# Optimization experiments

Hardware: AMD Instinct MI355X
Metric: run time of the kernel (lower is better)

## Reference

```python
import jax, jax.numpy as jnp
import numpy as np

B, DS, DM = 4, 64, 4096
NE, S = 1024, 2048


def setup_inputs() -> dict:
    key = jax.random.key(0)
    ks = jax.random.split(key, 9)
    std = 0.02
    return {
        "state": jax.random.normal(ks[0], (B, DS, DM), jnp.float32),
        "evicted_tokens": jax.random.normal(ks[1], (B, NE, DM), jnp.float32),
        "current_tokens": jax.random.normal(ks[2], (B, S, DM), jnp.float32),
        "W_key": std * jax.random.normal(ks[3], (DS, DM), jnp.float32),
        "W_beta_w": std * jax.random.normal(ks[4], (DS, DM), jnp.float32),
        "W_beta_b": jnp.zeros((DS,), jnp.float32),
        "W_query": std * jax.random.normal(ks[5], (DS, DM), jnp.float32),
        "gate_w": std * jax.random.normal(ks[6], (1, DM), jnp.float32),
        "gate_b": jnp.full((1,), -2.0, jnp.float32),  # gate_bias init
    }


def reference(state, evicted_tokens, current_tokens, W_key, W_beta_w, W_beta_b,
              W_query, gate_w, gate_b):
    # ---- compress: fold evicted tokens into SSM state ----
    # keys: [B, NE, DS]; softmax over the token axis (dim=1)
    keys = jnp.einsum('bnd,sd->bns', evicted_tokens, W_key)
    write_weights = jax.nn.softmax(keys, axis=1)
    # update: [B, DS, DM] = write_weights^T @ evicted_tokens
    update = jnp.einsum('bns,bnd->bsd', write_weights, evicted_tokens)
    summary = evicted_tokens.mean(axis=1)  # [B, DM]
    beta = jax.nn.sigmoid(summary @ W_beta_w.T + W_beta_b)  # [B, DS]
    new_state = beta[:, :, None] * state + update  # [B, DS, DM]
    # ---- query: gated linear-attention readout ----
    q = jnp.einsum('bld,sd->bls', current_tokens, W_query)  # [B, S, DS]
    retrieved = jnp.einsum('bls,bsd->bld', q, new_state)    # [B, S, DM]
    gate = jax.nn.sigmoid(current_tokens @ gate_w.T + gate_b)  # [B, S, 1]
    return gate * retrieved
```

## Files before the change

kernel.cpp:

```cpp
#include <hip/hip_runtime.h>

#define DM 4096
#define DSZ 64
#define NE 1024
#define SQ 2048
#define NB 4

typedef __attribute__((ext_vector_type(8))) short bf16x8;
typedef __attribute__((ext_vector_type(4))) float f32x4;

__device__ __forceinline__ unsigned f2bf(float f) {
  union { float f; unsigned u; } v; v.f = f;
  return (v.u + 0x7fffu + ((v.u >> 16) & 1u)) >> 16;
}
__device__ __forceinline__ unsigned pack2(float lo, float hi) {
  return f2bf(lo) | (f2bf(hi) << 16);
}

__device__ __forceinline__ void load8(const float* __restrict__ ap, const float* __restrict__ bp,
                                      float4& a0, float4& a1, float4& a2, float4& a3,
                                      float4& b0, float4& b1, float4& b2, float4& b3) {
  a0 = *(const float4*)(ap);      a1 = *(const float4*)(ap + 4);
  a2 = *(const float4*)(ap + 8);  a3 = *(const float4*)(ap + 12);
  b0 = *(const float4*)(bp);      b1 = *(const float4*)(bp + 4);
  b2 = *(const float4*)(bp + 8);  b3 = *(const float4*)(bp + 12);
}

__launch_bounds__(256)
__global__ void k_keys(const float* __restrict__ ev, const float* __restrict__ Wk,
                       float* __restrict__ keys_part) {
  __shared__ __align__(16) unsigned short As[2][64][72];
  __shared__ __align__(16) unsigned short Bs[2][64][72];
  const int bid = blockIdx.x;
  const int ks = bid & 7, mt = (bid >> 3) & 15, b = bid >> 7;
  const int n0 = mt * 64;
  const int t = threadIdx.x;
  const int w = t >> 6, m15 = t & 15, quad = (t & 63) >> 4;
  const int rowS = t >> 2, seg = (t & 3) * 16;

  f32x4 acc[4];
#pragma unroll
  for (int i = 0; i < 4; ++i) acc[i] = (f32x4){0.f, 0.f, 0.f, 0.f};

  const float* ap = ev + ((size_t)(b * NE + n0 + rowS)) * DM + ks * 512 + seg;
  const float* bp = Wk + (size_t)rowS * DM + ks * 512 + seg;

  float4 a0, a1, a2, a3, b0, b1, b2, b3;
  load8(ap, bp, a0, a1, a2, a3, b0, b1, b2, b3);
  int cur = 0;
  for (int ch = 0; ch < 8; ++ch) {
    *(uint4*)&As[cur][rowS][seg]     = (uint4){ pack2(a0.x,a0.y), pack2(a0.z,a0.w), pack2(a1.x,a1.y), pack2(a1.z,a1.w) };
    *(uint4*)&As[cur][rowS][seg + 8] = (uint4){ pack2(a2.x,a2.y), pack2(a2.z,a2.w), pack2(a3.x,a3.y), pack2(a3.z,a3.w) };
    *(uint4*)&Bs[cur][rowS][seg]     = (uint4){ pack2(b0.x,b0.y), pack2(b0.z,b0.w), pack2(b1.x,b1.y), pack2(b1.z,b1.w) };
    *(uint4*)&Bs[cur][rowS][seg + 8] = (uint4){ pack2(b2.x,b2.y), pack2(b2.z,b2.w), pack2(b3.x,b3.y), pack2(b3.z,b3.w) };
    __syncthreads();
    if (ch < 7) {
      ap += 64; bp += 64;
      load8(ap, bp, a0, a1, a2, a3, b0, b1, b2, b3);
    }
#pragma unroll
    for (int kk = 0; kk < 2; ++kk) {
      bf16x8 af = *(const bf16x8*)&As[cur][w * 16 + m15][kk * 32 + quad * 8];
#pragma unroll
      for (int tn = 0; tn < 4; ++tn) {
        bf16x8 bfr = *(const bf16x8*)&Bs[cur][tn * 16 + m15][kk * 32 + quad * 8];
        acc[tn] = __builtin_amdgcn_mfma_f32_16x16x32_bf16(af, bfr, acc[tn], 0, 0, 0);
      }
    }
    cur ^= 1;
  }
  const int n = n0 + w * 16 + quad * 4;
#pragma unroll
  for (int tn = 0; tn < 4; ++tn) {
    const int s = tn * 16 + m15;
    float4 v = { acc[tn][0], acc[tn][1], acc[tn][2], acc[tn][3] };
    *(float4*)&keys_part[(size_t)ks * (NB * DSZ * NE) + ((size_t)(b * DSZ + s)) * NE + n] = v;
  }
}

__launch_bounds__(256)
__global__ void k_sum(const float* __restrict__ ev, float* __restrict__ summary) {
  __shared__ float red[256];
  const int bid = blockIdx.x;
  const int b = bid >> 7, rem = bid & 127;
  const int d0 = (rem >> 1) * 64, half = rem & 1;
  const int t = threadIdx.x;
  const int dl = t & 63, g = t >> 6;
  float acc = 0.f;
  const float* p = ev + ((size_t)(b * NE + half * 512 + g * 128)) * DM + d0 + dl;
  for (int i = 0; i < 128; ++i) { acc += *p; p += DM; }
  red[t] = acc;
  __syncthreads();
  if (t < 64) {
    float tot = red[t] + red[t + 64] + red[t + 128] + red[t + 192];
    atomicAdd(&summary[b * DM + d0 + t], tot * (1.f / 1024.f));
  }
}

__launch_bounds__(256)
__global__ void k_beta(const float* __restrict__ summary, const float* __restrict__ Wbw,
                       const float* __restrict__ Wbb, float* __restrict__ beta) {
  __shared__ float wred[4];
  const int b = blockIdx.x >> 6, s = blockIdx.x & 63;
  const int t = threadIdx.x;
  const float* sp = summary + b * DM + t * 16;
  const float* wp = Wbw + (size_t)s * DM + t * 16;
  float acc = 0.f;
#pragma unroll
  for (int j = 0; j < 4; ++j) {
    float4 a  = *(const float4*)(sp + j * 4);
    float4 w4 = *(const float4*)(wp + j * 4);
    acc += a.x * w4.x + a.y * w4.y + a.z * w4.z + a.w * w4.w;
  }
#pragma unroll
  for (int off = 32; off > 0; off >>= 1) acc += __shfl_xor(acc, off);
  if ((t & 63) == 0) wred[t >> 6] = acc;
  __syncthreads();
  if (t == 0) {
    float x = wred[0] + wred[1] + wred[2] + wred[3] + Wbb[s];
    beta[b * DSZ + s] = 1.f / (1.f + expf(-x));
  }
}

__launch_bounds__(256)
__global__ void k_softmax(const float* __restrict__ keys_part, unsigned short* __restrict__ ww_t) {
  __shared__ float wred[8];
  const int b = blockIdx.x >> 6, s = blockIdx.x & 63;
  const int t = threadIdx.x;
  const size_t base = ((size_t)(b * DSZ + s)) * NE + t * 4;
  float4 k = {0.f, 0.f, 0.f, 0.f};
#pragma unroll
  for (int sl = 0; sl < 8; ++sl) {
    float4 p = *(const float4*)&keys_part[(size_t)sl * (NB * DSZ * NE) + base];
    k.x += p.x; k.y += p.y; k.z += p.z; k.w += p.w;
  }
  float m = fmaxf(fmaxf(k.x, k.y), fmaxf(k.z, k.w));
#pragma unroll
  for (int off = 32; off > 0; off >>= 1) m = fmaxf(m, __shfl_xor(m, off));
  if ((t & 63) == 0) wred[t >> 6] = m;
  __syncthreads();
  const float M = fmaxf(fmaxf(wred[0], wred[1]), fmaxf(wred[2], wred[3]));
  float4 e = { expf(k.x - M), expf(k.y - M), expf(k.z - M), expf(k.w - M) };
  float ss = e.x + e.y + e.z + e.w;
#pragma unroll
  for (int off = 32; off > 0; off >>= 1) ss += __shfl_xor(ss, off);
  if ((t & 63) == 0) wred[4 + (t >> 6)] = ss;
  __syncthreads();
  const float inv = 1.f / (wred[4] + wred[5] + wred[6] + wred[7]);
  ushort4 o = { (unsigned short)f2bf(e.x * inv), (unsigned short)f2bf(e.y * inv),
                (unsigned short)f2bf(e.z * inv), (unsigned short)f2bf(e.w * inv) };
  *(ushort4*)&ww_t[((size_t)(b * DSZ + s)) * NE + t * 4] = o;
}

__launch_bounds__(256)
__global__ void k_update(const float* __restrict__ ev, const float* __restrict__ state,
                         const float* __restrict__ beta, const unsigned short* __restrict__ ww_t,
                         unsigned short* __restrict__ ns_t) {
  __shared__ __align__(16) unsigned short Aw[2][64][72];
  __shared__ __align__(16) unsigned short Bt[2][32][72];
  const int bid = blockIdx.x;
  const int dt = bid & 127, b = bid >> 7;
  const int d0 = dt * 32;
  const int t = threadIdx.x;
  const int w = t >> 6, m15 = t & 15, quad = (t & 63) >> 4;
  const int rowS = t >> 2, seg = (t & 3) * 16;
  const int npair = (t & 31) * 2, dquad = (t >> 5) * 4;

  f32x4 acc[2];
#pragma unroll
  for (int i = 0; i < 2; ++i) acc[i] = (f32x4){0.f, 0.f, 0.f, 0.f};

  const unsigned short* wp = ww_t + ((size_t)(b * DSZ + rowS)) * NE + seg;
  const float* ep = ev + ((size_t)(b * NE + npair)) * DM + d0 + dquad;

  uint4 wa = *(const uint4*)(wp), wb = *(const uint4*)(wp + 8);
  float4 r0 = *(const float4*)(ep), r1 = *(const float4*)(ep + DM);
  int cur = 0;
  for (int ch = 0; ch < 16; ++ch) {
    *(uint4*)&Aw[cur][rowS][seg]     = wa;
    *(uint4*)&Aw[cur][rowS][seg + 8] = wb;
    *(unsigned*)&Bt[cur][dquad + 0][npair] = pack2(r0.x, r1.x);
    *(unsigned*)&Bt[cur][dquad + 1][npair] = pack2(r0.y, r1.y);
    *(unsigned*)&Bt[cur][dquad + 2][npair] = pack2(r0.z, r1.z);
    *(unsigned*)&Bt[cur][dquad + 3][npair] = pack2(r0.w, r1.w);
    __syncthreads();
    if (ch < 15) {
      wp += 64; ep += (size_t)64 * DM;
      wa = *(const uint4*)(wp); wb = *(const uint4*)(wp + 8);
      r0 = *(const float4*)(ep); r1 = *(const float4*)(ep + DM);
    }
#pragma unroll
    for (int kk = 0; kk < 2; ++kk) {
      bf16x8 af = *(const bf16x8*)&Aw[cur][w * 16 + m15][kk * 32 + quad * 8];
#pragma unroll
      for (int tn = 0; tn < 2; ++tn) {
        bf16x8 bfr = *(const bf16x8*)&Bt[cur][tn * 16 + m15][kk * 32 + quad * 8];
        acc[tn] = __builtin_amdgcn_mfma_f32_16x16x32_bf16(af, bfr, acc[tn], 0, 0, 0);
      }
    }
    cur ^= 1;
  }
  const int sbase = w * 16 + quad * 4;
#pragma unroll
  for (int tn = 0; tn < 2; ++tn) {
    const int d = d0 + tn * 16 + m15;
    float v[4];
#pragma unroll
    for (int r = 0; r < 4; ++r) {
      const int s = sbase + r;
      v[r] = beta[b * DSZ + s] * state[((size_t)(b * DSZ + s)) * DM + d] + acc[tn][r];
    }
    ushort4 o = { (unsigned short)f2bf(v[0]), (unsigned short)f2bf(v[1]),
                  (unsigned short)f2bf(v[2]), (unsigned short)f2bf(v[3]) };
    *(ushort4*)&ns_t[((size_t)(b * DM + d)) * DSZ + sbase] = o;
  }
}

__launch_bounds__(256)
__global__ void k_q(const float* __restrict__ cur_, const float* __restrict__ Wq,
                    const float* __restrict__ gate_w,
                    float* __restrict__ q_part, float* __restrict__ gate_acc) {
  __shared__ __align__(16) unsigned short As[2][64][72];
  __shared__ __align__(16) unsigned short Bs[2][64][72];
  __shared__ float gwAll[1024];
  __shared__ float gred[256];
  const int bid = blockIdx.x;
  const int ks = bid & 3, mt = (bid >> 2) & 31, b = bid >> 7;
  const int l0 = mt * 64;
  const int t = threadIdx.x;
  const int w = t >> 6, m15 = t & 15, quad = (t & 63) >> 4;
  const int rowS = t >> 2, seg = (t & 3) * 16;

  f32x4 acc[4];
#pragma unroll
  for (int i = 0; i < 4; ++i) acc[i] = (f32x4){0.f, 0.f, 0.f, 0.f};
  float gpart = 0.f;

  *(float4*)&gwAll[t * 4] = *(const float4*)(gate_w + ks * 1024 + t * 4);

  const float* ap = cur_ + ((size_t)(b * SQ + l0 + rowS)) * DM + ks * 1024 + seg;
  const float* bp = Wq + (size_t)rowS * DM + ks * 1024 + seg;

  float4 a0, a1, a2, a3, b0, b1, b2, b3;
  load8(ap, bp, a0, a1, a2, a3, b0, b1, b2, b3);
  int cur = 0;
  for (int ch = 0; ch < 16; ++ch) {
    *(uint4*)&As[cur][rowS][seg]     = (uint4){ pack2(a0.x,a0.y), pack2(a0.z,a0.w), pack2(a1.x,a1.y), pack2(a1.z,a1.w) };
    *(uint4*)&As[cur][rowS][seg + 8] = (uint4){ pack2(a2.x,a2.y), pack2(a2.z,a2.w), pack2(a3.x,a3.y), pack2(a3.z,a3.w) };
    *(uint4*)&Bs[cur][rowS][seg]     = (uint4){ pack2(b0.x,b0.y), pack2(b0.z,b0.w), pack2(b1.x,b1.y), pack2(b1.z,b1.w) };
    *(uint4*)&Bs[cur][rowS][seg + 8] = (uint4){ pack2(b2.x,b2.y), pack2(b2.z,b2.w), pack2(b3.x,b3.y), pack2(b3.z,b3.w) };
    __syncthreads();
    {
      const float* g = &gwAll[ch * 64 + seg];
      gpart += a0.x*g[0]  + a0.y*g[1]  + a0.z*g[2]  + a0.w*g[3]
             + a1.x*g[4]  + a1.y*g[5]  + a1.z*g[6]  + a1.w*g[7]
             + a2.x*g[8]  + a2.y*g[9]  + a2.z*g[10] + a2.w*g[11]
             + a3.x*g[12] + a3.y*g[13] + a3.z*g[14] + a3.w*g[15];
    }
    if (ch < 15) {
      ap += 64; bp += 64;
      load8(ap, bp, a0, a1, a2, a3, b0, b1, b2, b3);
    }
#pragma unroll
    for (int kk = 0; kk < 2; ++kk) {
      bf16x8 af = *(const bf16x8*)&As[cur][w * 16 + m15][kk * 32 + quad * 8];
#pragma unroll
      for (int tn = 0; tn < 4; ++tn) {
        bf16x8 bfr = *(const bf16x8*)&Bs[cur][tn * 16 + m15][kk * 32 + quad * 8];
        acc[tn] = __builtin_amdgcn_mfma_f32_16x16x32_bf16(af, bfr, acc[tn], 0, 0, 0);
      }
    }
    cur ^= 1;
  }
  const int lrow = l0 + w * 16 + quad * 4;
#pragma unroll
  for (int tn = 0; tn < 4; ++tn) {
#pragma unroll
    for (int r = 0; r < 4; ++r) {
      q_part[(size_t)ks * (NB * SQ * DSZ) + ((size_t)(b * SQ + lrow + r)) * DSZ + tn * 16 + m15] =
          acc[tn][r];
    }
  }
  gred[t] = gpart;
  __syncthreads();
  if (t < 64) {
    float tot = gred[4 * t] + gred[4 * t + 1] + gred[4 * t + 2] + gred[4 * t + 3];
    atomicAdd(&gate_acc[b * SQ + l0 + t], tot);
  }
}

__launch_bounds__(256)
__global__ void k_qcvt(const float* __restrict__ q_part, unsigned short* __restrict__ qbf) {
  const int i = (blockIdx.x * 256 + threadIdx.x) * 4;
  const int SL = NB * SQ * DSZ;
  float4 v0 = *(const float4*)&q_part[i];
  float4 v1 = *(const float4*)&q_part[i + SL];
  float4 v2 = *(const float4*)&q_part[i + 2 * SL];
  float4 v3 = *(const float4*)&q_part[i + 3 * SL];
  float x = v0.x + v1.x + v2.x + v3.x;
  float y = v0.y + v1.y + v2.y + v3.y;
  float z = v0.z + v1.z + v2.z + v3.z;
  float u = v0.w + v1.w + v2.w + v3.w;
  ushort4 o = { (unsigned short)f2bf(x), (unsigned short)f2bf(y),
                (unsigned short)f2bf(z), (unsigned short)f2bf(u) };
  *(ushort4*)&qbf[i] = o;
}

__launch_bounds__(256)
__global__ void k_out(const unsigned short* __restrict__ qbf, const unsigned short* __restrict__ ns_t,
                      const float* __restrict__ gate_acc, const float* __restrict__ gate_b,
                      float* __restrict__ out) {
  const int bid = blockIdx.x;
  const int dt = bid & 63, lt = (bid >> 6) & 31, b = bid >> 11;
  const int d0 = dt * 64, l0 = lt * 64;
  const int t = threadIdx.x;
  const int w = t >> 6, m15 = t & 15, quad = (t & 63) >> 4;
  const int la = l0 + w * 16 + m15;
  f32x4 acc[4];
#pragma unroll
  for (int i = 0; i < 4; ++i) acc[i] = (f32x4){0.f, 0.f, 0.f, 0.f};
#pragma unroll
  for (int kk = 0; kk < 2; ++kk) {
    bf16x8 af = *(const bf16x8*)&qbf[((size_t)(b * SQ + la)) * DSZ + kk * 32 + quad * 8];
#pragma unroll
    for (int tn = 0; tn < 4; ++tn) {
      const int d = d0 + tn * 16 + m15;
      bf16x8 bfr = *(const bf16x8*)&ns_t[((size_t)(b * DM + d)) * DSZ + kk * 32 + quad * 8];
      acc[tn] = __builtin_amdgcn_mfma_f32_16x16x32_bf16(af, bfr, acc[tn], 0, 0, 0);
    }
  }
  const float gb = gate_b[0];
  const int lbase = l0 + w * 16 + quad * 4;
  float g[4];
#pragma unroll
  for (int r = 0; r < 4; ++r)
    g[r] = 1.f / (1.f + expf(-(gate_acc[b * SQ + lbase + r] + gb)));
#pragma unroll
  for (int tn = 0; tn < 4; ++tn) {
    const int d = d0 + tn * 16 + m15;
#pragma unroll
    for (int r = 0; r < 4; ++r)
      out[((size_t)(b * SQ + lbase + r)) * DM + d] = g[r] * acc[tn][r];
  }
}

extern "C" void kernel_launch(void* const* d_in, const int* in_sizes, int n_in,
                              void* d_out, int out_size, void* d_ws, size_t ws_size,
                              hipStream_t stream) {
  const float* state   = (const float*)d_in[0];
  const float* evicted = (const float*)d_in[1];
  const float* current = (const float*)d_in[2];
  const float* Wkey    = (const float*)d_in[3];
  const float* Wbw     = (const float*)d_in[4];
  const float* Wbb     = (const float*)d_in[5];
  const float* Wq      = (const float*)d_in[6];
  const float* gate_w  = (const float*)d_in[7];
  const float* gate_b  = (const float*)d_in[8];
  float* out = (float*)d_out;

  float* f = (float*)d_ws;
  float* keys_part = f;
  float* q_part    = keys_part + 8 * 262144;
  float* summary   = q_part + 4 * 524288;
  float* gate_acc  = summary + 16384;
  float* beta      = gate_acc + 8192;
  unsigned short* ww_t = (unsigned short*)(beta + 256);
  unsigned short* qbf  = ww_t + 262144;
  unsigned short* ns_t = qbf + 524288;

  hipMemsetAsync(summary, 0, (16384 + 8192) * sizeof(float), stream);

  k_keys   <<<512,  256, 0, stream>>>(evicted, Wkey, keys_part);
  k_sum    <<<512,  256, 0, stream>>>(evicted, summary);
  k_beta   <<<256,  256, 0, stream>>>(summary, Wbw, Wbb, beta);
  k_softmax<<<256,  256, 0, stream>>>(keys_part, ww_t);
  k_update <<<512,  256, 0, stream>>>(evicted, state, beta, ww_t, ns_t);
  k_q      <<<512,  256, 0, stream>>>(current, Wq, gate_w, q_part, gate_acc);
  k_qcvt   <<<512,  256, 0, stream>>>(q_part, qbf);
  k_out    <<<8192, 256, 0, stream>>>(qbf, ns_t, gate_acc, gate_b, out);
}
```

Measured before the change: 386.0 us.

## Pre-convert inputs and weights to bf16 in separate passes fused with reductions

Adds conversion kernels that write bf16 copies of evicted tokens, current tokens and the key/query weights, folding the evicted-token mean and the gate dot product into those passes. The GEMM kernels then load bf16 directly, with no per-tile fp32-to-bf16 packing, and the standalone summary kernel is removed. This trades VALU conversion work inside the MFMA loops for extra global traffic: the bf16 copies of large activations are written and then re-read, and three launches are added.

```diff
diff --git a/kernel.cpp b/kernel.cpp
--- a/kernel.cpp
+++ b/kernel.cpp
@@ -17,17 +17,78 @@
   return f2bf(lo) | (f2bf(hi) << 16);
 }
 
-__device__ __forceinline__ void load8(const float* __restrict__ ap, const float* __restrict__ bp,
-                                      float4& a0, float4& a1, float4& a2, float4& a3,
-                                      float4& b0, float4& b1, float4& b2, float4& b3) {
-  a0 = *(const float4*)(ap);      a1 = *(const float4*)(ap + 4);
-  a2 = *(const float4*)(ap + 8);  a3 = *(const float4*)(ap + 12);
-  b0 = *(const float4*)(bp);      b1 = *(const float4*)(bp + 4);
-  b2 = *(const float4*)(bp + 8);  b3 = *(const float4*)(bp + 12);
-}
-
-__launch_bounds__(256)
-__global__ void k_keys(const float* __restrict__ ev, const float* __restrict__ Wk,
+__launch_bounds__(256)
+__global__ void k_cvt_ev(const float* __restrict__ ev, unsigned short* __restrict__ evb,
+                         float* __restrict__ summary) {
+  __shared__ float sred[4][512];
+  const int bid = blockIdx.x;
+  const int dsl = bid & 7, rgrp = (bid >> 3) & 15, b = bid >> 7;
+  const int t = threadIdx.x;
+  const int w = t >> 6, lane = t & 63;
+  const int d = dsl * 512 + lane * 8;
+  const size_t base = ((size_t)(b * NE + rgrp * 64 + w)) * DM + d;
+  float s0=0,s1=0,s2=0,s3=0,s4=0,s5=0,s6=0,s7=0;
+#pragma unroll 4
+  for (int it = 0; it < 16; ++it) {
+    const float* p = ev + base + (size_t)it * 4 * DM;
+    float4 v0 = *(const float4*)p;
+    float4 v1 = *(const float4*)(p + 4);
+    uint4 o = { pack2(v0.x,v0.y), pack2(v0.z,v0.w), pack2(v1.x,v1.y), pack2(v1.z,v1.w) };
+    *(uint4*)(evb + base + (size_t)it * 4 * DM) = o;
+    s0+=v0.x; s1+=v0.y; s2+=v0.z; s3+=v0.w; s4+=v1.x; s5+=v1.y; s6+=v1.z; s7+=v1.w;
+  }
+  sred[w][lane*8+0]=s0; sred[w][lane*8+1]=s1; sred[w][lane*8+2]=s2; sred[w][lane*8+3]=s3;
+  sred[w][lane*8+4]=s4; sred[w][lane*8+5]=s5; sred[w][lane*8+6]=s6; sred[w][lane*8+7]=s7;
+  __syncthreads();
+  const int di = t * 2;
+  float t0 = sred[0][di] + sred[1][di] + sred[2][di] + sred[3][di];
+  float t1 = sred[0][di+1] + sred[1][di+1] + sred[2][di+1] + sred[3][di+1];
+  atomicAdd(&summary[b * DM + dsl * 512 + di],     t0 * (1.f / 1024.f));
+  atomicAdd(&summary[b * DM + dsl * 512 + di + 1], t1 * (1.f / 1024.f));
+}
+
+__launch_bounds__(256)
+__global__ void k_cvt_cur(const float* __restrict__ cur, const float* __restrict__ gate_w,
+                          unsigned short* __restrict__ curb, float* __restrict__ gate_acc) {
+  const int bid = blockIdx.x;
+  const int dsl = bid & 7, rgrp = (bid >> 3) & 31, b = bid >> 8;
+  const int t = threadIdx.x;
+  const int w = t >> 6, lane = t & 63;
+  const int d = dsl * 512 + lane * 8;
+  const int l0 = rgrp * 64 + w;
+  float4 g0 = *(const float4*)(gate_w + d);
+  float4 g1 = *(const float4*)(gate_w + d + 4);
+  const size_t base = ((size_t)(b * SQ + l0)) * DM + d;
+#pragma unroll 4
+  for (int it = 0; it < 16; ++it) {
+    const float* p = cur + base + (size_t)it * 4 * DM;
+    float4 v0 = *(const float4*)p;
+    float4 v1 = *(const float4*)(p + 4);
+    uint4 o = { pack2(v0.x,v0.y), pack2(v0.z,v0.w), pack2(v1.x,v1.y), pack2(v1.z,v1.w) };
+    *(uint4*)(curb + base + (size_t)it * 4 * DM) = o;
+    float gp = v0.x*g0.x + v0.y*g0.y + v0.z*g0.z + v0.w*g0.w
+             + v1.x*g1.x + v1.y*g1.y + v1.z*g1.z + v1.w*g1.w;
+#pragma unroll
+    for (int off = 32; off > 0; off >>= 1) gp += __shfl_xor(gp, off);
+    if (lane == 0) atomicAdd(&gate_acc[b * SQ + l0 + it * 4], gp);
+  }
+}
+
+__launch_bounds__(256)
+__global__ void k_cvt_w(const float* __restrict__ Wk, const float* __restrict__ Wq,
+                        unsigned short* __restrict__ wkb, unsigned short* __restrict__ wqb) {
+  const int bid = blockIdx.x;
+  const float* src = (bid < 128) ? Wk : Wq;
+  unsigned short* dst = (bid < 128) ? wkb : wqb;
+  const int off = (bid & 127) * 2048 + threadIdx.x * 8;
+  float4 v0 = *(const float4*)(src + off);
+  float4 v1 = *(const float4*)(src + off + 4);
+  uint4 o = { pack2(v0.x,v0.y), pack2(v0.z,v0.w), pack2(v1.x,v1.y), pack2(v1.z,v1.w) };
+  *(uint4*)(dst + off) = o;
+}
+
+__launch_bounds__(256)
+__global__ void k_keys(const unsigned short* __restrict__ evb, const unsigned short* __restrict__ wkb,
                        float* __restrict__ keys_part) {
   __shared__ __align__(16) unsigned short As[2][64][72];
   __shared__ __align__(16) unsigned short Bs[2][64][72];
@@ -42,21 +103,22 @@
 #pragma unroll
   for (int i = 0; i < 4; ++i) acc[i] = (f32x4){0.f, 0.f, 0.f, 0.f};
 
-  const float* ap = ev + ((size_t)(b * NE + n0 + rowS)) * DM + ks * 512 + seg;
-  const float* bp = Wk + (size_t)rowS * DM + ks * 512 + seg;
-
-  float4 a0, a1, a2, a3, b0, b1, b2, b3;
-  load8(ap, bp, a0, a1, a2, a3, b0, b1, b2, b3);
+  const unsigned short* ap = evb + ((size_t)(b * NE + n0 + rowS)) * DM + ks * 512 + seg;
+  const unsigned short* bp = wkb + (size_t)rowS * DM + ks * 512 + seg;
+
+  uint4 a0 = *(const uint4*)ap, a1 = *(const uint4*)(ap + 8);
+  uint4 b0 = *(const uint4*)bp, b1 = *(const uint4*)(bp + 8);
   int cur = 0;
   for (int ch = 0; ch < 8; ++ch) {
-    *(uint4*)&As[cur][rowS][seg]     = (uint4){ pack2(a0.x,a0.y), pack2(a0.z,a0.w), pack2(a1.x,a1.y), pack2(a1.z,a1.w) };
-    *(uint4*)&As[cur][rowS][seg + 8] = (uint4){ pack2(a2.x,a2.y), pack2(a2.z,a2.w), pack2(a3.x,a3.y), pack2(a3.z,a3.w) };
-    *(uint4*)&Bs[cur][rowS][seg]     = (uint4){ pack2(b0.x,b0.y), pack2(b0.z,b0.w), pack2(b1.x,b1.y), pack2(b1.z,b1.w) };
-    *(uint4*)&Bs[cur][rowS][seg + 8] = (uint4){ pack2(b2.x,b2.y), pack2(b2.z,b2.w), pack2(b3.x,b3.y), pack2(b3.z,b3.w) };
+    *(uint4*)&As[cur][rowS][seg]     = a0;
+    *(uint4*)&As[cur][rowS][seg + 8] = a1;
+    *(uint4*)&Bs[cur][rowS][seg]     = b0;
+    *(uint4*)&Bs[cur][rowS][seg + 8] = b1;
     __syncthreads();
     if (ch < 7) {
       ap += 64; bp += 64;
-      load8(ap, bp, a0, a1, a2, a3, b0, b1, b2, b3);
+      a0 = *(const uint4*)ap; a1 = *(const uint4*)(ap + 8);
+      b0 = *(const uint4*)bp; b1 = *(const uint4*)(bp + 8);
     }
 #pragma unroll
     for (int kk = 0; kk < 2; ++kk) {
@@ -75,25 +137,6 @@
     const int s = tn * 16 + m15;
     float4 v = { acc[tn][0], acc[tn][1], acc[tn][2], acc[tn][3] };
     *(float4*)&keys_part[(size_t)ks * (NB * DSZ * NE) + ((size_t)(b * DSZ + s)) * NE + n] = v;
-  }
-}
-
-__launch_bounds__(256)
-__global__ void k_sum(const float* __restrict__ ev, float* __restrict__ summary) {
-  __shared__ float red[256];
-  const int bid = blockIdx.x;
-  const int b = bid >> 7, rem = bid & 127;
-  const int d0 = (rem >> 1) * 64, half = rem & 1;
-  const int t = threadIdx.x;
-  const int dl = t & 63, g = t >> 6;
-  float acc = 0.f;
-  const float* p = ev + ((size_t)(b * NE + half * 512 + g * 128)) * DM + d0 + dl;
-  for (int i = 0; i < 128; ++i) { acc += *p; p += DM; }
-  red[t] = acc;
-  __syncthreads();
-  if (t < 64) {
-    float tot = red[t] + red[t + 64] + red[t + 128] + red[t + 192];
-    atomicAdd(&summary[b * DM + d0 + t], tot * (1.f / 1024.f));
   }
 }
 
@@ -153,7 +196,7 @@
 }
 
 __launch_bounds__(256)
-__global__ void k_update(const float* __restrict__ ev, const float* __restrict__ state,
+__global__ void k_update(const unsigned short* __restrict__ evb, const float* __restrict__ state,
                          const float* __restrict__ beta, const unsigned short* __restrict__ ww_t,
                          unsigned short* __restrict__ ns_t) {
   __shared__ __align__(16) unsigned short Aw[2][64][72];
@@ -171,23 +214,23 @@
   for (int i = 0; i < 2; ++i) acc[i] = (f32x4){0.f, 0.f, 0.f, 0.f};
 
   const unsigned short* wp = ww_t + ((size_t)(b * DSZ + rowS)) * NE + seg;
-  const float* ep = ev + ((size_t)(b * NE + npair)) * DM + d0 + dquad;
+  const unsigned short* ep = evb + ((size_t)(b * NE + npair)) * DM + d0 + dquad;
 
   uint4 wa = *(const uint4*)(wp), wb = *(const uint4*)(wp + 8);
-  float4 r0 = *(const float4*)(ep), r1 = *(const float4*)(ep + DM);
+  uint2 r0 = *(const uint2*)(ep), r1 = *(const uint2*)(ep + DM);
   int cur = 0;
   for (int ch = 0; ch < 16; ++ch) {
     *(uint4*)&Aw[cur][rowS][seg]     = wa;
     *(uint4*)&Aw[cur][rowS][seg + 8] = wb;
-    *(unsigned*)&Bt[cur][dquad + 0][npair] = pack2(r0.x, r1.x);
-    *(unsigned*)&Bt[cur][dquad + 1][npair] = pack2(r0.y, r1.y);
-    *(unsigned*)&Bt[cur][dquad + 2][npair] = pack2(r0.z, r1.z);
-    *(unsigned*)&Bt[cur][dquad + 3][npair] = pack2(r0.w, r1.w);
+    *(unsigned*)&Bt[cur][dquad + 0][npair] = (r0.x & 0xffffu) | (r1.x << 16);
+    *(unsigned*)&Bt[cur][dquad + 1][npair] = (r0.x >> 16) | (r1.x & 0xffff0000u);
+    *(unsigned*)&Bt[cur][dquad + 2][npair] = (r0.y & 0xffffu) | (r1.y << 16);
+    *(unsigned*)&Bt[cur][dquad + 3][npair] = (r0.y >> 16) | (r1.y & 0xffff0000u);
     __syncthreads();
     if (ch < 15) {
       wp += 64; ep += (size_t)64 * DM;
       wa = *(const uint4*)(wp); wb = *(const uint4*)(wp + 8);
-      r0 = *(const float4*)(ep); r1 = *(const float4*)(ep + DM);
+      r0 = *(const uint2*)(ep); r1 = *(const uint2*)(ep + DM);
     }
 #pragma unroll
     for (int kk = 0; kk < 2; ++kk) {
@@ -217,13 +260,10 @@
 }
 
 __launch_bounds__(256)
-__global__ void k_q(const float* __restrict__ cur_, const float* __restrict__ Wq,
-                    const float* __restrict__ gate_w,
-                    float* __restrict__ q_part, float* __restrict__ gate_acc) {
+__global__ void k_q(const unsigned short* __restrict__ curb, const unsigned short* __restrict__ wqb,
+                    float* __restrict__ q_part) {
   __shared__ __align__(16) unsigned short As[2][64][72];
   __shared__ __align__(16) unsigned short Bs[2][64][72];
-  __shared__ float gwAll[1024];
-  __shared__ float gred[256];
   const int bid = blockIdx.x;
   const int ks = bid & 3, mt = (bid >> 2) & 31, b = bid >> 7;
   const int l0 = mt * 64;
@@ -234,32 +274,23 @@
   f32x4 acc[4];
 #pragma unroll
   for (int i = 0; i < 4; ++i) acc[i] = (f32x4){0.f, 0.f, 0.f, 0.f};
-  float gpart = 0.f;
-
-  *(float4*)&gwAll[t * 4] = *(const float4*)(gate_w + ks * 1024 + t * 4);
-
-  const float* ap = cur_ + ((size_t)(b * SQ + l0 + rowS)) * DM + ks * 1024 + seg;
-  const float* bp = Wq + (size_t)rowS * DM + ks * 1024 + seg;
-
-  float4 a0, a1, a2, a3, b0, b1, b2, b3;
-  load8(ap, bp, a0, a1, a2, a3, b0, b1, b2, b3);
+
+  const unsigned short* ap = curb + ((size_t)(b * SQ + l0 + rowS)) * DM + ks * 1024 + seg;
+  const unsigned short* bp = wqb + (size_t)rowS * DM + ks * 1024 + seg;
+
+  uint4 a0 = *(const uint4*)ap, a1 = *(const uint4*)(ap + 8);
+  uint4 b0 = *(const uint4*)bp, b1 = *(const uint4*)(bp + 8);
   int cur = 0;
   for (int ch = 0; ch < 16; ++ch) {
-    *(uint4*)&As[cur][rowS][seg]     = (uint4){ pack2(a0.x,a0.y), pack2(a0.z,a0.w), pack2(a1.x,a1.y), pack2(a1.z,a1.w) };
-    *(uint4*)&As[cur][rowS][seg + 8] = (uint4){ pack2(a2.x,a2.y), pack2(a2.z,a2.w), pack2(a3.x,a3.y), pack2(a3.z,a3.w) };
-    *(uint4*)&Bs[cur][rowS][seg]     = (uint4){ pack2(b0.x,b0.y), pack2(b0.z,b0.w), pack2(b1.x,b1.y), pack2(b1.z,b1.w) };
-    *(uint4*)&Bs[cur][rowS][seg + 8] = (uint4){ pack2(b2.x,b2.y), pack2(b2.z,b2.w), pack2(b3.x,b3.y), pack2(b3.z,b3.w) };
+    *(uint4*)&As[cur][rowS][seg]     = a0;
+    *(uint4*)&As[cur][rowS][seg + 8] = a1;
+    *(uint4*)&Bs[cur][rowS][seg]     = b0;
+    *(uint4*)&Bs[cur][rowS][seg + 8] = b1;
     __syncthreads();
-    {
-      const float* g = &gwAll[ch * 64 + seg];
-      gpart += a0.x*g[0]  + a0.y*g[1]  + a0.z*g[2]  + a0.w*g[3]
-             + a1.x*g[4]  + a1.y*g[5]  + a1.z*g[6]  + a1.w*g[7]
-             + a2.x*g[8]  + a2.y*g[9]  + a2.z*g[10] + a2.w*g[11]
-             + a3.x*g[12] + a3.y*g[13] + a3.z*g[14] + a3.w*g[15];
-    }
     if (ch < 15) {
       ap += 64; bp += 64;
-      load8(ap, bp, a0, a1, a2, a3, b0, b1, b2, b3);
+      a0 = *(const uint4*)ap; a1 = *(const uint4*)(ap + 8);
+      b0 = *(const uint4*)bp; b1 = *(const uint4*)(bp + 8);
     }
 #pragma unroll
     for (int kk = 0; kk < 2; ++kk) {
@@ -280,12 +311,6 @@
       q_part[(size_t)ks * (NB * SQ * DSZ) + ((size_t)(b * SQ + lrow + r)) * DSZ + tn * 16 + m15] =
           acc[tn][r];
     }
-  }
-  gred[t] = gpart;
-  __syncthreads();
-  if (t < 64) {
-    float tot = gred[4 * t] + gred[4 * t + 1] + gred[4 * t + 2] + gred[4 * t + 3];
-    atomicAdd(&gate_acc[b * SQ + l0 + t], tot);
   }
 }
 
@@ -367,15 +392,21 @@
   unsigned short* ww_t = (unsigned short*)(beta + 256);
   unsigned short* qbf  = ww_t + 262144;
   unsigned short* ns_t = qbf + 524288;
+  unsigned short* evb  = ns_t + 1048576;
+  unsigned short* curb = evb + 16777216;
+  unsigned short* wkb  = curb + 33554432;
+  unsigned short* wqb  = wkb + 262144;
 
   hipMemsetAsync(summary, 0, (16384 + 8192) * sizeof(float), stream);
 
-  k_keys   <<<512,  256, 0, stream>>>(evicted, Wkey, keys_part);
-  k_sum    <<<512,  256, 0, stream>>>(evicted, summary);
+  k_cvt_w  <<<256,  256, 0, stream>>>(Wkey, Wq, wkb, wqb);
+  k_cvt_ev <<<512,  256, 0, stream>>>(evicted, evb, summary);
+  k_cvt_cur<<<1024, 256, 0, stream>>>(current, gate_w, curb, gate_acc);
+  k_keys   <<<512,  256, 0, stream>>>(evb, wkb, keys_part);
   k_beta   <<<256,  256, 0, stream>>>(summary, Wbw, Wbb, beta);
   k_softmax<<<256,  256, 0, stream>>>(keys_part, ww_t);
-  k_update <<<512,  256, 0, stream>>>(evicted, state, beta, ww_t, ns_t);
-  k_q      <<<512,  256, 0, stream>>>(current, Wq, gate_w, q_part, gate_acc);
+  k_update <<<512,  256, 0, stream>>>(evb, state, beta, ww_t, ns_t);
+  k_q      <<<512,  256, 0, stream>>>(curb, wqb, q_part);
   k_qcvt   <<<512,  256, 0, stream>>>(q_part, qbf);
   k_out    <<<8192, 256, 0, stream>>>(qbf, ns_t, gate_acc, gate_b, out);
 }
```

After: 402.9 us. +4.4%, slower.

## Fuse summary, beta, softmax and q conversion into neighbouring kernels; reuse bf16 evicted copy

Applied to the files above, without the earlier changes.

The column-sum for the summary now happens inside the keys GEMM, reading from shared-memory tiles, so the separate summary kernel no longer reads the evicted tokens a second time. The keys kernel also writes a bf16 copy of the evicted tokens, which the update kernel reads at half the bytes. Beta is folded into the softmax kernel, and the q slice reduction plus bf16 conversion moves into the output kernel's prologue. Launch count drops from eight to five, at the cost of an extra bf16 write of the evicted tensor and the q partials being re-read once per d-tile in the output kernel. The summary is now computed from bf16-rounded values, which adds a small precision loss.

```diff
diff --git a/kernel.cpp b/kernel.cpp
--- a/kernel.cpp
+++ b/kernel.cpp
@@ -15,6 +15,9 @@
 }
 __device__ __forceinline__ unsigned pack2(float lo, float hi) {
   return f2bf(lo) | (f2bf(hi) << 16);
+}
+__device__ __forceinline__ float bf2f(unsigned short h) {
+  union { unsigned u; float f; } v; v.u = ((unsigned)h) << 16; return v.f;
 }
 
 __device__ __forceinline__ void load8(const float* __restrict__ ap, const float* __restrict__ bp,
@@ -28,15 +31,18 @@
 
 __launch_bounds__(256)
 __global__ void k_keys(const float* __restrict__ ev, const float* __restrict__ Wk,
-                       float* __restrict__ keys_part) {
+                       float* __restrict__ keys_part, unsigned short* __restrict__ evb,
+                       float* __restrict__ summary) {
   __shared__ __align__(16) unsigned short As[2][64][72];
   __shared__ __align__(16) unsigned short Bs[2][64][72];
+  __shared__ float csum[8][4][64];
   const int bid = blockIdx.x;
   const int ks = bid & 7, mt = (bid >> 3) & 15, b = bid >> 7;
   const int n0 = mt * 64;
   const int t = threadIdx.x;
   const int w = t >> 6, m15 = t & 15, quad = (t & 63) >> 4;
   const int rowS = t >> 2, seg = (t & 3) * 16;
+  const int ccol = t & 63, cgrp = t >> 6;
 
   f32x4 acc[4];
 #pragma unroll
@@ -44,19 +50,30 @@
 
   const float* ap = ev + ((size_t)(b * NE + n0 + rowS)) * DM + ks * 512 + seg;
   const float* bp = Wk + (size_t)rowS * DM + ks * 512 + seg;
+  unsigned short* evp = evb + ((size_t)(b * NE + n0 + rowS)) * DM + ks * 512 + seg;
 
   float4 a0, a1, a2, a3, b0, b1, b2, b3;
   load8(ap, bp, a0, a1, a2, a3, b0, b1, b2, b3);
   int cur = 0;
   for (int ch = 0; ch < 8; ++ch) {
-    *(uint4*)&As[cur][rowS][seg]     = (uint4){ pack2(a0.x,a0.y), pack2(a0.z,a0.w), pack2(a1.x,a1.y), pack2(a1.z,a1.w) };
-    *(uint4*)&As[cur][rowS][seg + 8] = (uint4){ pack2(a2.x,a2.y), pack2(a2.z,a2.w), pack2(a3.x,a3.y), pack2(a3.z,a3.w) };
+    uint4 pa0 = { pack2(a0.x,a0.y), pack2(a0.z,a0.w), pack2(a1.x,a1.y), pack2(a1.z,a1.w) };
+    uint4 pa1 = { pack2(a2.x,a2.y), pack2(a2.z,a2.w), pack2(a3.x,a3.y), pack2(a3.z,a3.w) };
+    *(uint4*)&As[cur][rowS][seg]     = pa0;
+    *(uint4*)&As[cur][rowS][seg + 8] = pa1;
     *(uint4*)&Bs[cur][rowS][seg]     = (uint4){ pack2(b0.x,b0.y), pack2(b0.z,b0.w), pack2(b1.x,b1.y), pack2(b1.z,b1.w) };
     *(uint4*)&Bs[cur][rowS][seg + 8] = (uint4){ pack2(b2.x,b2.y), pack2(b2.z,b2.w), pack2(b3.x,b3.y), pack2(b3.z,b3.w) };
+    *(uint4*)(evp)     = pa0;
+    *(uint4*)(evp + 8) = pa1;
     __syncthreads();
     if (ch < 7) {
-      ap += 64; bp += 64;
+      ap += 64; bp += 64; evp += 64;
       load8(ap, bp, a0, a1, a2, a3, b0, b1, b2, b3);
+    }
+    {
+      float cs = 0.f;
+#pragma unroll
+      for (int r = 0; r < 16; ++r) cs += bf2f(As[cur][cgrp * 16 + r][ccol]);
+      csum[ch][cgrp][ccol] = cs;
     }
 #pragma unroll
     for (int kk = 0; kk < 2; ++kk) {
@@ -76,57 +93,38 @@
     float4 v = { acc[tn][0], acc[tn][1], acc[tn][2], acc[tn][3] };
     *(float4*)&keys_part[(size_t)ks * (NB * DSZ * NE) + ((size_t)(b * DSZ + s)) * NE + n] = v;
   }
-}
-
-__launch_bounds__(256)
-__global__ void k_sum(const float* __restrict__ ev, float* __restrict__ summary) {
-  __shared__ float red[256];
-  const int bid = blockIdx.x;
-  const int b = bid >> 7, rem = bid & 127;
-  const int d0 = (rem >> 1) * 64, half = rem & 1;
-  const int t = threadIdx.x;
-  const int dl = t & 63, g = t >> 6;
-  float acc = 0.f;
-  const float* p = ev + ((size_t)(b * NE + half * 512 + g * 128)) * DM + d0 + dl;
-  for (int i = 0; i < 128; ++i) { acc += *p; p += DM; }
-  red[t] = acc;
   __syncthreads();
   if (t < 64) {
-    float tot = red[t] + red[t + 64] + red[t + 128] + red[t + 192];
-    atomicAdd(&summary[b * DM + d0 + t], tot * (1.f / 1024.f));
-  }
-}
-
-__launch_bounds__(256)
-__global__ void k_beta(const float* __restrict__ summary, const float* __restrict__ Wbw,
-                       const float* __restrict__ Wbb, float* __restrict__ beta) {
-  __shared__ float wred[4];
-  const int b = blockIdx.x >> 6, s = blockIdx.x & 63;
-  const int t = threadIdx.x;
-  const float* sp = summary + b * DM + t * 16;
-  const float* wp = Wbw + (size_t)s * DM + t * 16;
-  float acc = 0.f;
-#pragma unroll
-  for (int j = 0; j < 4; ++j) {
-    float4 a  = *(const float4*)(sp + j * 4);
-    float4 w4 = *(const float4*)(wp + j * 4);
-    acc += a.x * w4.x + a.y * w4.y + a.z * w4.z + a.w * w4.w;
-  }
-#pragma unroll
-  for (int off = 32; off > 0; off >>= 1) acc += __shfl_xor(acc, off);
-  if ((t & 63) == 0) wred[t >> 6] = acc;
-  __syncthreads();
-  if (t == 0) {
-    float x = wred[0] + wred[1] + wred[2] + wred[3] + Wbb[s];
-    beta[b * DSZ + s] = 1.f / (1.f + expf(-x));
-  }
-}
-
-__launch_bounds__(256)
-__global__ void k_softmax(const float* __restrict__ keys_part, unsigned short* __restrict__ ww_t) {
+#pragma unroll
+    for (int c2 = 0; c2 < 8; ++c2) {
+      float ssum = csum[c2][0][t] + csum[c2][1][t] + csum[c2][2][t] + csum[c2][3][t];
+      atomicAdd(&summary[b * DM + ks * 512 + c2 * 64 + t], ssum * (1.f / 1024.f));
+    }
+  }
+}
+
+__launch_bounds__(256)
+__global__ void k_bs(const float* __restrict__ summary, const float* __restrict__ Wbw,
+                     const float* __restrict__ Wbb, const float* __restrict__ keys_part,
+                     float* __restrict__ beta, unsigned short* __restrict__ ww_t) {
+  __shared__ float wredb[4];
   __shared__ float wred[8];
   const int b = blockIdx.x >> 6, s = blockIdx.x & 63;
   const int t = threadIdx.x;
+  {
+    const float* sp = summary + b * DM + t * 16;
+    const float* wp = Wbw + (size_t)s * DM + t * 16;
+    float acc = 0.f;
+#pragma unroll
+    for (int j = 0; j < 4; ++j) {
+      float4 a  = *(const float4*)(sp + j * 4);
+      float4 w4 = *(const float4*)(wp + j * 4);
+      acc += a.x * w4.x + a.y * w4.y + a.z * w4.z + a.w * w4.w;
+    }
+#pragma unroll
+    for (int off = 32; off > 0; off >>= 1) acc += __shfl_xor(acc, off);
+    if ((t & 63) == 0) wredb[t >> 6] = acc;
+  }
   const size_t base = ((size_t)(b * DSZ + s)) * NE + t * 4;
   float4 k = {0.f, 0.f, 0.f, 0.f};
 #pragma unroll
@@ -150,10 +148,14 @@
   ushort4 o = { (unsigned short)f2bf(e.x * inv), (unsigned short)f2bf(e.y * inv),
                 (unsigned short)f2bf(e.z * inv), (unsigned short)f2bf(e.w * inv) };
   *(ushort4*)&ww_t[((size_t)(b * DSZ + s)) * NE + t * 4] = o;
-}
-
-__launch_bounds__(256)
-__global__ void k_update(const float* __restrict__ ev, const float* __restrict__ state,
+  if (t == 0) {
+    float x = wredb[0] + wredb[1] + wredb[2] + wredb[3] + Wbb[s];
+    beta[b * DSZ + s] = 1.f / (1.f + expf(-x));
+  }
+}
+
+__launch_bounds__(256)
+__global__ void k_update(const unsigned short* __restrict__ evb, const float* __restrict__ state,
                          const float* __restrict__ beta, const unsigned short* __restrict__ ww_t,
                          unsigned short* __restrict__ ns_t) {
   __shared__ __align__(16) unsigned short Aw[2][64][72];
@@ -171,23 +173,23 @@
   for (int i = 0; i < 2; ++i) acc[i] = (f32x4){0.f, 0.f, 0.f, 0.f};
 
   const unsigned short* wp = ww_t + ((size_t)(b * DSZ + rowS)) * NE + seg;
-  const float* ep = ev + ((size_t)(b * NE + npair)) * DM + d0 + dquad;
+  const unsigned short* ep = evb + ((size_t)(b * NE + npair)) * DM + d0 + dquad;
 
   uint4 wa = *(const uint4*)(wp), wb = *(const uint4*)(wp + 8);
-  float4 r0 = *(const float4*)(ep), r1 = *(const float4*)(ep + DM);
+  uint2 r0 = *(const uint2*)(ep), r1 = *(const uint2*)(ep + DM);
   int cur = 0;
   for (int ch = 0; ch < 16; ++ch) {
     *(uint4*)&Aw[cur][rowS][seg]     = wa;
     *(uint4*)&Aw[cur][rowS][seg + 8] = wb;
-    *(unsigned*)&Bt[cur][dquad + 0][npair] = pack2(r0.x, r1.x);
-    *(unsigned*)&Bt[cur][dquad + 1][npair] = pack2(r0.y, r1.y);
-    *(unsigned*)&Bt[cur][dquad + 2][npair] = pack2(r0.z, r1.z);
-    *(unsigned*)&Bt[cur][dquad + 3][npair] = pack2(r0.w, r1.w);
+    *(unsigned*)&Bt[cur][dquad + 0][npair] = (r0.x & 0xffffu) | (r1.x << 16);
+    *(unsigned*)&Bt[cur][dquad + 1][npair] = (r0.x >> 16) | (r1.x & 0xffff0000u);
+    *(unsigned*)&Bt[cur][dquad + 2][npair] = (r0.y & 0xffffu) | (r1.y << 16);
+    *(unsigned*)&Bt[cur][dquad + 3][npair] = (r0.y >> 16) | (r1.y & 0xffff0000u);
     __syncthreads();
     if (ch < 15) {
       wp += 64; ep += (size_t)64 * DM;
       wa = *(const uint4*)(wp); wb = *(const uint4*)(wp + 8);
-      r0 = *(const float4*)(ep); r1 = *(const float4*)(ep + DM);
+      r0 = *(const uint2*)(ep); r1 = *(const uint2*)(ep + DM);
     }
 #pragma unroll
     for (int kk = 0; kk < 2; ++kk) {
@@ -290,38 +292,42 @@
 }
 
 __launch_bounds__(256)
-__global__ void k_qcvt(const float* __restrict__ q_part, unsigned short* __restrict__ qbf) {
-  const int i = (blockIdx.x * 256 + threadIdx.x) * 4;
-  const int SL = NB * SQ * DSZ;
-  float4 v0 = *(const float4*)&q_part[i];
-  float4 v1 = *(const float4*)&q_part[i + SL];
-  float4 v2 = *(const float4*)&q_part[i + 2 * SL];
-  float4 v3 = *(const float4*)&q_part[i + 3 * SL];
-  float x = v0.x + v1.x + v2.x + v3.x;
-  float y = v0.y + v1.y + v2.y + v3.y;
-  float z = v0.z + v1.z + v2.z + v3.z;
-  float u = v0.w + v1.w + v2.w + v3.w;
-  ushort4 o = { (unsigned short)f2bf(x), (unsigned short)f2bf(y),
-                (unsigned short)f2bf(z), (unsigned short)f2bf(u) };
-  *(ushort4*)&qbf[i] = o;
-}
-
-__launch_bounds__(256)
-__global__ void k_out(const unsigned short* __restrict__ qbf, const unsigned short* __restrict__ ns_t,
+__global__ void k_out(const float* __restrict__ q_part, const unsigned short* __restrict__ ns_t,
                       const float* __restrict__ gate_acc, const float* __restrict__ gate_b,
                       float* __restrict__ out) {
+  __shared__ __align__(16) unsigned short Qs[64][72];
   const int bid = blockIdx.x;
   const int dt = bid & 63, lt = (bid >> 6) & 31, b = bid >> 11;
   const int d0 = dt * 64, l0 = lt * 64;
   const int t = threadIdx.x;
   const int w = t >> 6, m15 = t & 15, quad = (t & 63) >> 4;
-  const int la = l0 + w * 16 + m15;
+  const int rowS = t >> 2, seg = (t & 3) * 16;
+  {
+    const int SL = NB * SQ * DSZ;
+    const float* qp = q_part + ((size_t)(b * SQ + l0 + rowS)) * DSZ + seg;
+    float4 s0 = {0,0,0,0}, s1 = s0, s2 = s0, s3 = s0;
+#pragma unroll
+    for (int sl = 0; sl < 4; ++sl) {
+      const float* p = qp + (size_t)sl * SL;
+      float4 u0 = *(const float4*)(p);
+      float4 u1 = *(const float4*)(p + 4);
+      float4 u2 = *(const float4*)(p + 8);
+      float4 u3 = *(const float4*)(p + 12);
+      s0.x += u0.x; s0.y += u0.y; s0.z += u0.z; s0.w += u0.w;
+      s1.x += u1.x; s1.y += u1.y; s1.z += u1.z; s1.w += u1.w;
+      s2.x += u2.x; s2.y += u2.y; s2.z += u2.z; s2.w += u2.w;
+      s3.x += u3.x; s3.y += u3.y; s3.z += u3.z; s3.w += u3.w;
+    }
+    *(uint4*)&Qs[rowS][seg]     = (uint4){ pack2(s0.x,s0.y), pack2(s0.z,s0.w), pack2(s1.x,s1.y), pack2(s1.z,s1.w) };
+    *(uint4*)&Qs[rowS][seg + 8] = (uint4){ pack2(s2.x,s2.y), pack2(s2.z,s2.w), pack2(s3.x,s3.y), pack2(s3.z,s3.w) };
+  }
+  __syncthreads();
   f32x4 acc[4];
 #pragma unroll
   for (int i = 0; i < 4; ++i) acc[i] = (f32x4){0.f, 0.f, 0.f, 0.f};
 #pragma unroll
   for (int kk = 0; kk < 2; ++kk) {
-    bf16x8 af = *(const bf16x8*)&qbf[((size_t)(b * SQ + la)) * DSZ + kk * 32 + quad * 8];
+    bf16x8 af = *(const bf16x8*)&Qs[w * 16 + m15][kk * 32 + quad * 8];
 #pragma unroll
     for (int tn = 0; tn < 4; ++tn) {
       const int d = d0 + tn * 16 + m15;
@@ -365,17 +371,14 @@
   float* gate_acc  = summary + 16384;
   float* beta      = gate_acc + 8192;
   unsigned short* ww_t = (unsigned short*)(beta + 256);
-  unsigned short* qbf  = ww_t + 262144;
-  unsigned short* ns_t = qbf + 524288;
+  unsigned short* ns_t = ww_t + 262144;
+  unsigned short* evb  = ns_t + 1048576;
 
   hipMemsetAsync(summary, 0, (16384 + 8192) * sizeof(float), stream);
 
-  k_keys   <<<512,  256, 0, stream>>>(evicted, Wkey, keys_part);
-  k_sum    <<<512,  256, 0, stream>>>(evicted, summary);
-  k_beta   <<<256,  256, 0, stream>>>(summary, Wbw, Wbb, beta);
-  k_softmax<<<256,  256, 0, stream>>>(keys_part, ww_t);
-  k_update <<<512,  256, 0, stream>>>(evicted, state, beta, ww_t, ns_t);
+  k_keys   <<<512,  256, 0, stream>>>(evicted, Wkey, keys_part, evb, summary);
   k_q      <<<512,  256, 0, stream>>>(current, Wq, gate_w, q_part, gate_acc);
-  k_qcvt   <<<512,  256, 0, stream>>>(q_part, qbf);
-  k_out    <<<8192, 256, 0, stream>>>(qbf, ns_t, gate_acc, gate_b, out);
-}
+  k_bs     <<<256,  256, 0, stream>>>(summary, Wbw, Wbb, keys_part, beta, ww_t);
+  k_update <<<512,  256, 0, stream>>>(evb, state, beta, ww_t, ns_t);
+  k_out    <<<8192, 256, 0, stream>>>(q_part, ns_t, gate_acc, gate_b, out);
+}
```

New measurement: 391.7 us. No clear change (+1.5%).
